# Optimization experiments

Measured on AMD Instinct MI355X. Metric: run time of the kernel, lower is better.

## Reference

```python
import jax, jax.numpy as jnp
import numpy as np

PAD = 0
NEG_INF = -1e30

B, P, Q, D = 32, 4096, 64, 128  # batch, passage len, question len, nhid


def setup_inputs() -> dict:
    key = jax.random.key(0)
    k1, k2, k3, k4, k5, k6 = jax.random.split(key, 6)
    return {
        "tensor_H": jax.random.normal(k1, (B, P, D), dtype=jnp.float32),
        "tensor_U": jax.random.normal(k2, (B, Q, D), dtype=jnp.float32),
        "M": jax.random.normal(k3, (B, P, D), dtype=jnp.float32),
        "sentence_word_rep": jax.random.randint(k4, (B, P), 0, 10000, dtype=jnp.int64),
        "W_attn": jax.random.normal(k5, (D, D), dtype=jnp.float32) / np.sqrt(D),
        "W_cls": jax.random.normal(k6, (5 * D, 2), dtype=jnp.float32) / np.sqrt(5 * D),
    }


def reference(tensor_H, tensor_U, M, sentence_word_rep, W_attn, W_cls):
    # Matrix attention (bilinear): S[b,p,q] = h_p^T W u_q  -> (B, P, Q)
    S = jnp.einsum("bpd,de,bqe->bpq", tensor_H, W_attn, tensor_U)
    # context-to-query: softmax over question axis, then bmm with U
    c2q = jnp.einsum("bpq,bqd->bpd", jax.nn.softmax(S, axis=2), tensor_U)
    # query-to-context: softmax over passage axis of row-max, weighted sum of H
    b_attn = jax.nn.softmax(jnp.max(S, axis=2), axis=-1)        # (B, P)
    q2c = jnp.einsum("bp,bpd->bd", b_attn, tensor_H)[:, None, :]  # (B, 1, D) broadcast over P
    # G = [H; c2q; H*c2q; H*q2c] -> (B, P, 4D); G_M = [G; M] -> (B, P, 5D)
    G_M = jnp.concatenate(
        [tensor_H, c2q, tensor_H * c2q, tensor_H * q2c, M], axis=2
    )
    # masked max-pool over passage positions (mask where token == PAD)
    pad_mask = (sentence_word_rep == PAD)[:, :, None]           # (B, P, 1)
    pooled = jnp.max(jnp.where(pad_mask, NEG_INF, G_M), axis=1)  # (B, 5D)
    # final linear classifier (no bias)
    return pooled @ W_cls                                        # (B, 2)
```

## Files before the change

### kernel.cpp

```cpp
#include <hip/hip_runtime.h>

#define B_ 32
#define P_ 4096
#define Q_ 64
#define D_ 128

#define PART_STRIDE 772
#define NCHUNK 32
#define CHUNK_ROWS 128
#define TWS_BYTES (96*16384)

typedef __attribute__((ext_vector_type(8))) short bf16x8;
typedef __attribute__((ext_vector_type(4))) float f32x4;

__device__ __forceinline__ unsigned int asu(float x) { return __float_as_uint(x); }
__device__ __forceinline__ float asf(unsigned int x) { return __uint_as_float(x); }

__global__ __launch_bounds__(256) void k_T(const float* __restrict__ U,
                                           const float* __restrict__ W,
                                           char* __restrict__ Tws) {
  __shared__ float Wl[128*132];
  __shared__ float Ul[8*128];
  const int b = blockIdx.x >> 3, qc = blockIdx.x & 7;
  const int t = threadIdx.x;
#pragma unroll
  for (int k = 0; k < 16; ++k) {
    int i = t*4 + k*1024;
    float4 wv = *(const float4*)(W + i);
    int d = i >> 7, e = i & 127;
    *(float4*)(&Wl[d*132 + e]) = wv;
  }
  {
    int i = t*4;
    int q = i >> 7, e = i & 127;
    *(float4*)(&Ul[q*128 + e]) =
        *(const float4*)(U + ((size_t)(b*Q_ + qc*8 + q))*D_ + e);
  }
  __syncthreads();
  const int d = t & 127, qhalf = t >> 7;
  char* Thi = Tws + b*16384;
  char* Tlo = Tws + 32*16384 + b*16384;
  char* Utl = Tws + 64*16384 + b*16384;
#pragma unroll
  for (int pass = 0; pass < 4; ++pass) {
    const int ql = pass*2 + qhalf;
    const int qg = qc*8 + ql;
    float acc = 0.f;
#pragma unroll
    for (int e = 0; e < 128; e += 4) {
      float4 wv = *(float4*)(&Wl[d*132 + e]);
      float4 uv = *(float4*)(&Ul[ql*128 + e]);
      acc += wv.x*uv.x + wv.y*uv.y + wv.z*uv.z + wv.w*uv.w;
    }
    unsigned int au = asu(acc);
    unsigned short hs = (unsigned short)(au >> 16);
    float lo = acc - asf(au & 0xFFFF0000u);
    unsigned short ls = (unsigned short)(asu(lo) >> 16);
    int ta = (qg*256 + 2*d) ^ ((qg & 7) << 4);
    *(unsigned short*)(Thi + ta) = hs;
    *(unsigned short*)(Tlo + ta) = ls;
    float uval = Ul[ql*128 + d];
    int ua = (d*128 + 2*qg) ^ ((d & 7) << 4);
    *(unsigned short*)(Utl + ua) = (unsigned short)(asu(uval) >> 16);
  }
}

__global__ __launch_bounds__(512, 8) void k_main(
    const float* __restrict__ H, const float* __restrict__ M,
    const int* __restrict__ tok, const char* __restrict__ Tws,
    float* __restrict__ part) {
  __shared__ __align__(16) char Pl[16384];
  __shared__ float mrow[128];
  __shared__ float rzrow[128];
  __shared__ float prow[128];
  __shared__ int   tkl[128];

  const int bid = blockIdx.x;
  const int b = bid >> 5, chunk = bid & 31;
  const int t = threadIdx.x, wv = t >> 6, l = t & 63;
  const int r15 = l & 15, g4 = l >> 4;
  const char* Thi = Tws + b*16384;
  const char* Tlo = Tws + 32*16384 + b*16384;
  const char* Utl = Tws + 64*16384 + b*16384;

  if (t < 128) tkl[t] = tok[b*P_ + chunk*CHUNK_ROWS + t];

  const int rowB = b*P_ + chunk*CHUNK_ROWS;

  {
    const int lrow0 = wv*16;
    f32x4 sacc[4];
#pragma unroll
    for (int qt = 0; qt < 4; ++qt) sacc[qt] = (f32x4){0.f, 0.f, 0.f, 0.f};
    const float* Arow = H + (size_t)(rowB + lrow0 + r15)*D_;
#pragma unroll
    for (int ks = 0; ks < 4; ++ks) {
      const float* ap = Arow + ks*32 + g4*8;
      float4 fa = *(const float4*)(ap);
      float4 fb = *(const float4*)(ap + 4);
      union { bf16x8 v; unsigned int u[4]; } Ah, Al;
      {
        unsigned int a0 = asu(fa.x), a1 = asu(fa.y), a2 = asu(fa.z), a3 = asu(fa.w);
        unsigned int c0 = asu(fb.x), c1 = asu(fb.y), c2 = asu(fb.z), c3 = asu(fb.w);
        Ah.u[0] = (a1 & 0xFFFF0000u) | (a0 >> 16);
        Ah.u[1] = (a3 & 0xFFFF0000u) | (a2 >> 16);
        Ah.u[2] = (c1 & 0xFFFF0000u) | (c0 >> 16);
        Ah.u[3] = (c3 & 0xFFFF0000u) | (c2 >> 16);
        float p0 = fa.x - asf(a0 & 0xFFFF0000u);
        float p1 = fa.y - asf(a1 & 0xFFFF0000u);
        float p2 = fa.z - asf(a2 & 0xFFFF0000u);
        float p3 = fa.w - asf(a3 & 0xFFFF0000u);
        float p4 = fb.x - asf(c0 & 0xFFFF0000u);
        float p5 = fb.y - asf(c1 & 0xFFFF0000u);
        float p6 = fb.z - asf(c2 & 0xFFFF0000u);
        float p7 = fb.w - asf(c3 & 0xFFFF0000u);
        Al.u[0] = (asu(p1) & 0xFFFF0000u) | (asu(p0) >> 16);
        Al.u[1] = (asu(p3) & 0xFFFF0000u) | (asu(p2) >> 16);
        Al.u[2] = (asu(p5) & 0xFFFF0000u) | (asu(p4) >> 16);
        Al.u[3] = (asu(p7) & 0xFFFF0000u) | (asu(p6) >> 16);
      }
#pragma unroll
      for (int qt = 0; qt < 4; ++qt) {
        int q = qt*16 + r15;
        int off = (q*256 + ks*64 + g4*16) ^ ((q & 7) << 4);
        bf16x8 bh = *(const bf16x8*)(Thi + off);
        bf16x8 bl = *(const bf16x8*)(Tlo + off);
        sacc[qt] = __builtin_amdgcn_mfma_f32_16x16x32_bf16(Al.v, bh, sacc[qt], 0, 0, 0);
        sacc[qt] = __builtin_amdgcn_mfma_f32_16x16x32_bf16(Ah.v, bl, sacc[qt], 0, 0, 0);
        sacc[qt] = __builtin_amdgcn_mfma_f32_16x16x32_bf16(Ah.v, bh, sacc[qt], 0, 0, 0);
      }
    }
    float m[4];
#pragma unroll
    for (int j = 0; j < 4; ++j)
      m[j] = fmaxf(fmaxf(sacc[0][j], sacc[1][j]), fmaxf(sacc[2][j], sacc[3][j]));
#pragma unroll
    for (int off = 1; off <= 8; off <<= 1)
#pragma unroll
      for (int j = 0; j < 4; ++j) m[j] = fmaxf(m[j], __shfl_xor(m[j], off));
    float Zp[4] = {0.f, 0.f, 0.f, 0.f};
#pragma unroll
    for (int qt = 0; qt < 4; ++qt)
#pragma unroll
      for (int j = 0; j < 4; ++j) {
        float e = __expf(sacc[qt][j] - m[j]);
        Zp[j] += e;
        int p = lrow0 + g4*4 + j, q = qt*16 + r15;
        int off = (p*128 + 2*q) ^ ((p & 7) << 4);
        *(unsigned short*)(Pl + off) = (unsigned short)(asu(e) >> 16);
      }
#pragma unroll
    for (int off = 1; off <= 8; off <<= 1)
#pragma unroll
      for (int j = 0; j < 4; ++j) Zp[j] += __shfl_xor(Zp[j], off);
    if (r15 == 0) {
#pragma unroll
      for (int j = 0; j < 4; ++j) {
        mrow[lrow0 + g4*4 + j]  = m[j];
        rzrow[lrow0 + g4*4 + j] = __builtin_amdgcn_rcpf(Zp[j]);
      }
    }
  }
  __syncthreads();

  float m0 = mrow[l], m1 = mrow[l + 64];
  float Lm = fmaxf(m0, m1);
#pragma unroll
  for (int off = 1; off <= 32; off <<= 1) Lm = fmaxf(Lm, __shfl_xor(Lm, off));
  float ssum = __expf(m0 - Lm) + __expf(m1 - Lm);
#pragma unroll
  for (int off = 1; off <= 32; off <<= 1) ssum += __shfl_xor(ssum, off);
  if (t < 128) prow[t] = __expf(mrow[t] - Lm);
  __syncthreads();

  const int dd = wv*16 + r15;
  bf16x8 bu0 = *(const bf16x8*)(Utl + ((dd*128 +  0 + g4*16) ^ ((dd & 7) << 4)));
  bf16x8 bu1 = *(const bf16x8*)(Utl + ((dd*128 + 64 + g4*16) ^ ((dd & 7) << 4)));

  float v = 0.f, xH = -3.0e38f, nH = 3.0e38f;
  float xC = -3.0e38f, xHC = -3.0e38f, xM = -3.0e38f;
#pragma unroll
  for (int rti = 0; rti < 8; ++rti) {
    const int rt = (rti + wv) & 7;
    f32x4 pv = (f32x4){0.f, 0.f, 0.f, 0.f};
    {
      int pr0 = rt*16 + r15;
      bf16x8 a0 = *(bf16x8*)(Pl + ((pr0*128 +  0 + g4*16) ^ ((r15 & 7) << 4)));
      bf16x8 a1 = *(bf16x8*)(Pl + ((pr0*128 + 64 + g4*16) ^ ((r15 & 7) << 4)));
      pv = __builtin_amdgcn_mfma_f32_16x16x32_bf16(a0, bu0, pv, 0, 0, 0);
      pv = __builtin_amdgcn_mfma_f32_16x16x32_bf16(a1, bu1, pv, 0, 0, 0);
    }
    const float* Hrow = H + (size_t)(rowB + rt*16 + g4*4)*D_ + dd;
    const float* Mrow = M + (size_t)(rowB + rt*16 + g4*4)*D_ + dd;
#pragma unroll
    for (int j = 0; j < 4; ++j) {
      const int row = rt*16 + g4*4 + j;
      const int tkv = tkl[row];
      const float bmax = tkv ? 0.f : -1.0e38f;
      const float bmin = tkv ? 0.f : 1.0e38f;
      float pr = prow[row];
      float h  = Hrow[(size_t)j*D_];
      float mv = Mrow[(size_t)j*D_];
      float c  = pv[j] * rzrow[row];
      v   += pr*h;
      xH   = fmaxf(xH,  h + bmax);
      nH   = fminf(nH,  h + bmin);
      xC   = fmaxf(xC,  c + bmax);
      xHC  = fmaxf(xHC, h*c + bmax);
      xM   = fmaxf(xM,  mv + bmax);
    }
  }
#pragma unroll
  for (int off = 16; off <= 32; off <<= 1) {
    v   += __shfl_xor(v, off);
    xH   = fmaxf(xH,  __shfl_xor(xH,  off));
    nH   = fminf(nH,  __shfl_xor(nH,  off));
    xC   = fmaxf(xC,  __shfl_xor(xC,  off));
    xHC  = fmaxf(xHC, __shfl_xor(xHC, off));
    xM   = fmaxf(xM,  __shfl_xor(xM,  off));
  }
  float* pp = part + (size_t)bid*PART_STRIDE;
  if (t == 0) { pp[0] = Lm; pp[1] = ssum; }
  if (g4 == 0) {
    pp[2 + dd]   = v;
    pp[130 + dd] = xH;
    pp[258 + dd] = nH;
    pp[386 + dd] = xC;
    pp[514 + dd] = xHC;
    pp[642 + dd] = xM;
  }
}

__global__ __launch_bounds__(128) void k_final(const float* __restrict__ part,
                                               const float* __restrict__ Wc,
                                               float* __restrict__ out) {
  __shared__ float pooled[640];
  __shared__ float r0s[2], r1s[2];
  const int b = blockIdx.x, t = threadIdx.x;
  const float* pb = part + (size_t)b*NCHUNK*PART_STRIDE;
  float L = -3.0e38f;
#pragma unroll
  for (int c = 0; c < NCHUNK; ++c) L = fmaxf(L, pb[c*PART_STRIDE]);
  float S = 0.f, V = 0.f;
  float mh = -3.0e38f, nh = 3.0e38f, mc = -3.0e38f, mhc = -3.0e38f, mm = -3.0e38f;
#pragma unroll
  for (int c = 0; c < NCHUNK; ++c) {
    const float* p = pb + c*PART_STRIDE;
    float e = __expf(p[0] - L);
    S += p[1]*e;
    V += p[2 + t]*e;
    mh  = fmaxf(mh,  p[130 + t]);
    nh  = fminf(nh,  p[258 + t]);
    mc  = fmaxf(mc,  p[386 + t]);
    mhc = fmaxf(mhc, p[514 + t]);
    mm  = fmaxf(mm,  p[642 + t]);
  }
  float q2c = V / S;
  pooled[t]       = mh;
  pooled[128 + t] = mc;
  pooled[256 + t] = mhc;
  pooled[384 + t] = (q2c >= 0.f) ? q2c*mh : q2c*nh;
  pooled[512 + t] = mm;
  __syncthreads();
  float a0 = 0.f, a1 = 0.f;
#pragma unroll
  for (int k = t; k < 640; k += 128) {
    float pv = pooled[k];
    a0 += pv*Wc[k*2 + 0];
    a1 += pv*Wc[k*2 + 1];
  }
#pragma unroll
  for (int off = 32; off; off >>= 1) {
    a0 += __shfl_xor(a0, off);
    a1 += __shfl_xor(a1, off);
  }
  if ((t & 63) == 0) { r0s[t >> 6] = a0; r1s[t >> 6] = a1; }
  __syncthreads();
  if (t == 0) {
    out[b*2 + 0] = r0s[0] + r0s[1];
    out[b*2 + 1] = r1s[0] + r1s[1];
  }
}

extern "C" void kernel_launch(void* const* d_in, const int* in_sizes, int n_in,
                              void* d_out, int out_size, void* d_ws, size_t ws_size,
                              hipStream_t stream) {
  const float* H   = (const float*)d_in[0];
  const float* U   = (const float*)d_in[1];
  const float* M   = (const float*)d_in[2];
  const int*   tok = (const int*)d_in[3];
  const float* Wa  = (const float*)d_in[4];
  const float* Wc  = (const float*)d_in[5];
  float* out = (float*)d_out;
  char* wsc = (char*)d_ws;
  char* Tws = wsc;
  float* part = (float*)(wsc + TWS_BYTES);

  hipLaunchKernelGGL(k_T,     dim3(256),        dim3(256), 0, stream, U, Wa, Tws);
  hipLaunchKernelGGL(k_main,  dim3(B_*NCHUNK),  dim3(512), 0, stream, H, M, tok, Tws, part);
  hipLaunchKernelGGL(k_final, dim3(B_),         dim3(128), 0, stream, part, Wc, out);
}
```

Baseline: 65.10 us.

## Halve chunk size to 64 rows, use 256-thread blocks with two d-columns per lane

Splits each batch's passage into 64 chunks of 64 rows, so twice as many blocks run with 256 threads each. In the second phase each lane now covers two output columns and reuses the same P fragments for two MFMAs. Per-row mask, probability and reciprocal values are precomputed into shared arrays and read as float4 vectors. The aim is better occupancy and more parallelism, at the cost of twice as many partial records for k_final to reduce.

```diff
diff --git a/kernel.cpp b/kernel.cpp
--- a/kernel.cpp
+++ b/kernel.cpp
@@ -6,8 +6,8 @@
 #define D_ 128
 
 #define PART_STRIDE 772
-#define NCHUNK 32
-#define CHUNK_ROWS 128
+#define NCHUNK 64
+#define CHUNK_ROWS 64
 #define TWS_BYTES (96*16384)
 
 typedef __attribute__((ext_vector_type(8))) short bf16x8;
@@ -65,55 +65,56 @@
   }
 }
 
-__global__ __launch_bounds__(512, 8) void k_main(
+__global__ __launch_bounds__(256, 8) void k_main(
     const float* __restrict__ H, const float* __restrict__ M,
     const int* __restrict__ tok, const char* __restrict__ Tws,
     float* __restrict__ part) {
-  __shared__ __align__(16) char Pl[16384];
-  __shared__ float mrow[128];
-  __shared__ float rzrow[128];
-  __shared__ float prow[128];
-  __shared__ int   tkl[128];
+  __shared__ __align__(16) char Pl[8192];
+  __shared__ __align__(16) float mrow[64];
+  __shared__ __align__(16) float rzrow[64];
+  __shared__ __align__(16) float prow[64];
+  __shared__ __align__(16) float bm[64];
+  __shared__ int tkl[64];
 
   const int bid = blockIdx.x;
-  const int b = bid >> 5, chunk = bid & 31;
+  const int b = bid >> 6, chunk = bid & 63;
   const int t = threadIdx.x, wv = t >> 6, l = t & 63;
   const int r15 = l & 15, g4 = l >> 4;
-  const char* Thi = Tws + b*16384;
-  const char* Tlo = Tws + 32*16384 + b*16384;
-  const char* Utl = Tws + 64*16384 + b*16384;
-
-  if (t < 128) tkl[t] = tok[b*P_ + chunk*CHUNK_ROWS + t];
+  const char* Thi_g = Tws + b*16384;
+  const char* Tlo_g = Tws + 32*16384 + b*16384;
+  const char* Utl   = Tws + 64*16384 + b*16384;
+
+  if (t < 64) tkl[t] = tok[b*P_ + chunk*CHUNK_ROWS + t];
 
   const int rowB = b*P_ + chunk*CHUNK_ROWS;
 
   {
     const int lrow0 = wv*16;
+    const float* Arow = H + (size_t)(rowB + lrow0 + r15)*D_;
     f32x4 sacc[4];
 #pragma unroll
     for (int qt = 0; qt < 4; ++qt) sacc[qt] = (f32x4){0.f, 0.f, 0.f, 0.f};
-    const float* Arow = H + (size_t)(rowB + lrow0 + r15)*D_;
 #pragma unroll
     for (int ks = 0; ks < 4; ++ks) {
       const float* ap = Arow + ks*32 + g4*8;
-      float4 fa = *(const float4*)(ap);
-      float4 fb = *(const float4*)(ap + 4);
+      f32x4 fa = *(const f32x4*)(ap);
+      f32x4 fb = *(const f32x4*)(ap + 4);
       union { bf16x8 v; unsigned int u[4]; } Ah, Al;
       {
-        unsigned int a0 = asu(fa.x), a1 = asu(fa.y), a2 = asu(fa.z), a3 = asu(fa.w);
-        unsigned int c0 = asu(fb.x), c1 = asu(fb.y), c2 = asu(fb.z), c3 = asu(fb.w);
+        unsigned int a0 = asu(fa[0]), a1 = asu(fa[1]), a2 = asu(fa[2]), a3 = asu(fa[3]);
+        unsigned int c0 = asu(fb[0]), c1 = asu(fb[1]), c2 = asu(fb[2]), c3 = asu(fb[3]);
         Ah.u[0] = (a1 & 0xFFFF0000u) | (a0 >> 16);
         Ah.u[1] = (a3 & 0xFFFF0000u) | (a2 >> 16);
         Ah.u[2] = (c1 & 0xFFFF0000u) | (c0 >> 16);
         Ah.u[3] = (c3 & 0xFFFF0000u) | (c2 >> 16);
-        float p0 = fa.x - asf(a0 & 0xFFFF0000u);
-        float p1 = fa.y - asf(a1 & 0xFFFF0000u);
-        float p2 = fa.z - asf(a2 & 0xFFFF0000u);
-        float p3 = fa.w - asf(a3 & 0xFFFF0000u);
-        float p4 = fb.x - asf(c0 & 0xFFFF0000u);
-        float p5 = fb.y - asf(c1 & 0xFFFF0000u);
-        float p6 = fb.z - asf(c2 & 0xFFFF0000u);
-        float p7 = fb.w - asf(c3 & 0xFFFF0000u);
+        float p0 = fa[0] - asf(a0 & 0xFFFF0000u);
+        float p1 = fa[1] - asf(a1 & 0xFFFF0000u);
+        float p2 = fa[2] - asf(a2 & 0xFFFF0000u);
+        float p3 = fa[3] - asf(a3 & 0xFFFF0000u);
+        float p4 = fb[0] - asf(c0 & 0xFFFF0000u);
+        float p5 = fb[1] - asf(c1 & 0xFFFF0000u);
+        float p6 = fb[2] - asf(c2 & 0xFFFF0000u);
+        float p7 = fb[3] - asf(c3 & 0xFFFF0000u);
         Al.u[0] = (asu(p1) & 0xFFFF0000u) | (asu(p0) >> 16);
         Al.u[1] = (asu(p3) & 0xFFFF0000u) | (asu(p2) >> 16);
         Al.u[2] = (asu(p5) & 0xFFFF0000u) | (asu(p4) >> 16);
@@ -123,8 +124,8 @@
       for (int qt = 0; qt < 4; ++qt) {
         int q = qt*16 + r15;
         int off = (q*256 + ks*64 + g4*16) ^ ((q & 7) << 4);
-        bf16x8 bh = *(const bf16x8*)(Thi + off);
-        bf16x8 bl = *(const bf16x8*)(Tlo + off);
+        bf16x8 bh = *(const bf16x8*)(Thi_g + off);
+        bf16x8 bl = *(const bf16x8*)(Tlo_g + off);
         sacc[qt] = __builtin_amdgcn_mfma_f32_16x16x32_bf16(Al.v, bh, sacc[qt], 0, 0, 0);
         sacc[qt] = __builtin_amdgcn_mfma_f32_16x16x32_bf16(Ah.v, bl, sacc[qt], 0, 0, 0);
         sacc[qt] = __builtin_amdgcn_mfma_f32_16x16x32_bf16(Ah.v, bh, sacc[qt], 0, 0, 0);
@@ -163,71 +164,86 @@
   }
   __syncthreads();
 
-  float m0 = mrow[l], m1 = mrow[l + 64];
-  float Lm = fmaxf(m0, m1);
+  float m0 = mrow[l];
+  float Lm = m0;
 #pragma unroll
   for (int off = 1; off <= 32; off <<= 1) Lm = fmaxf(Lm, __shfl_xor(Lm, off));
-  float ssum = __expf(m0 - Lm) + __expf(m1 - Lm);
+  float ssum = __expf(m0 - Lm);
 #pragma unroll
   for (int off = 1; off <= 32; off <<= 1) ssum += __shfl_xor(ssum, off);
-  if (t < 128) prow[t] = __expf(mrow[t] - Lm);
-  __syncthreads();
-
-  const int dd = wv*16 + r15;
-  bf16x8 bu0 = *(const bf16x8*)(Utl + ((dd*128 +  0 + g4*16) ^ ((dd & 7) << 4)));
-  bf16x8 bu1 = *(const bf16x8*)(Utl + ((dd*128 + 64 + g4*16) ^ ((dd & 7) << 4)));
-
-  float v = 0.f, xH = -3.0e38f, nH = 3.0e38f;
-  float xC = -3.0e38f, xHC = -3.0e38f, xM = -3.0e38f;
-#pragma unroll
-  for (int rti = 0; rti < 8; ++rti) {
-    const int rt = (rti + wv) & 7;
-    f32x4 pv = (f32x4){0.f, 0.f, 0.f, 0.f};
+  if (t < 64) {
+    prow[t] = __expf(mrow[t] - Lm);
+    bm[t]   = tkl[t] ? 0.f : -1.0e38f;
+  }
+  __syncthreads();
+
+  const int dd0 = wv*32 + r15;
+  const int dd1 = dd0 + 16;
+  bf16x8 bu00 = *(const bf16x8*)(Utl + ((dd0*128 +  0 + g4*16) ^ ((dd0 & 7) << 4)));
+  bf16x8 bu01 = *(const bf16x8*)(Utl + ((dd0*128 + 64 + g4*16) ^ ((dd0 & 7) << 4)));
+  bf16x8 bu10 = *(const bf16x8*)(Utl + ((dd1*128 +  0 + g4*16) ^ ((dd1 & 7) << 4)));
+  bf16x8 bu11 = *(const bf16x8*)(Utl + ((dd1*128 + 64 + g4*16) ^ ((dd1 & 7) << 4)));
+
+  float v0 = 0.f, v1 = 0.f;
+  float xH0 = -3.0e38f, xH1 = -3.0e38f, nH0 = 3.0e38f, nH1 = 3.0e38f;
+  float xC0 = -3.0e38f, xC1 = -3.0e38f, xHC0 = -3.0e38f, xHC1 = -3.0e38f;
+  float xM0 = -3.0e38f, xM1 = -3.0e38f;
+#pragma unroll
+  for (int rti = 0; rti < 4; ++rti) {
+    const int rt = (rti + wv) & 3;
+    f32x4 pv0 = (f32x4){0.f, 0.f, 0.f, 0.f};
+    f32x4 pv1 = (f32x4){0.f, 0.f, 0.f, 0.f};
     {
       int pr0 = rt*16 + r15;
       bf16x8 a0 = *(bf16x8*)(Pl + ((pr0*128 +  0 + g4*16) ^ ((r15 & 7) << 4)));
       bf16x8 a1 = *(bf16x8*)(Pl + ((pr0*128 + 64 + g4*16) ^ ((r15 & 7) << 4)));
-      pv = __builtin_amdgcn_mfma_f32_16x16x32_bf16(a0, bu0, pv, 0, 0, 0);
-      pv = __builtin_amdgcn_mfma_f32_16x16x32_bf16(a1, bu1, pv, 0, 0, 0);
-    }
-    const float* Hrow = H + (size_t)(rowB + rt*16 + g4*4)*D_ + dd;
-    const float* Mrow = M + (size_t)(rowB + rt*16 + g4*4)*D_ + dd;
+      pv0 = __builtin_amdgcn_mfma_f32_16x16x32_bf16(a0, bu00, pv0, 0, 0, 0);
+      pv0 = __builtin_amdgcn_mfma_f32_16x16x32_bf16(a1, bu01, pv0, 0, 0, 0);
+      pv1 = __builtin_amdgcn_mfma_f32_16x16x32_bf16(a0, bu10, pv1, 0, 0, 0);
+      pv1 = __builtin_amdgcn_mfma_f32_16x16x32_bf16(a1, bu11, pv1, 0, 0, 0);
+    }
+    const int rg = rt*16 + g4*4;
+    const float* Hrow = H + (size_t)(rowB + rg)*D_;
+    const float* Mrow = M + (size_t)(rowB + rg)*D_;
+    f32x4 prw = *(const f32x4*)&prow[rg];
+    f32x4 rzw = *(const f32x4*)&rzrow[rg];
+    f32x4 bmw = *(const f32x4*)&bm[rg];
 #pragma unroll
     for (int j = 0; j < 4; ++j) {
-      const int row = rt*16 + g4*4 + j;
-      const int tkv = tkl[row];
-      const float bmax = tkv ? 0.f : -1.0e38f;
-      const float bmin = tkv ? 0.f : 1.0e38f;
-      float pr = prow[row];
-      float h  = Hrow[(size_t)j*D_];
-      float mv = Mrow[(size_t)j*D_];
-      float c  = pv[j] * rzrow[row];
-      v   += pr*h;
-      xH   = fmaxf(xH,  h + bmax);
-      nH   = fminf(nH,  h + bmin);
-      xC   = fmaxf(xC,  c + bmax);
-      xHC  = fmaxf(xHC, h*c + bmax);
-      xM   = fmaxf(xM,  mv + bmax);
+      const float bmax = bmw[j];
+      const float bmin = -bmax;
+      float h0 = Hrow[(size_t)j*D_ + dd0];
+      float h1 = Hrow[(size_t)j*D_ + dd1];
+      float mv0 = Mrow[(size_t)j*D_ + dd0];
+      float mv1 = Mrow[(size_t)j*D_ + dd1];
+      float c0 = pv0[j] * rzw[j];
+      float c1 = pv1[j] * rzw[j];
+      v0   += prw[j]*h0;             v1   += prw[j]*h1;
+      xH0   = fmaxf(xH0,  h0 + bmax);  xH1   = fmaxf(xH1,  h1 + bmax);
+      nH0   = fminf(nH0,  h0 + bmin);  nH1   = fminf(nH1,  h1 + bmin);
+      xC0   = fmaxf(xC0,  c0 + bmax);  xC1   = fmaxf(xC1,  c1 + bmax);
+      xHC0  = fmaxf(xHC0, h0*c0 + bmax); xHC1 = fmaxf(xHC1, h1*c1 + bmax);
+      xM0   = fmaxf(xM0,  mv0 + bmax); xM1   = fmaxf(xM1,  mv1 + bmax);
     }
   }
 #pragma unroll
   for (int off = 16; off <= 32; off <<= 1) {
-    v   += __shfl_xor(v, off);
-    xH   = fmaxf(xH,  __shfl_xor(xH,  off));
-    nH   = fminf(nH,  __shfl_xor(nH,  off));
-    xC   = fmaxf(xC,  __shfl_xor(xC,  off));
-    xHC  = fmaxf(xHC, __shfl_xor(xHC, off));
-    xM   = fmaxf(xM,  __shfl_xor(xM,  off));
+    v0   += __shfl_xor(v0, off);            v1   += __shfl_xor(v1, off);
+    xH0   = fmaxf(xH0,  __shfl_xor(xH0,  off)); xH1 = fmaxf(xH1, __shfl_xor(xH1, off));
+    nH0   = fminf(nH0,  __shfl_xor(nH0,  off)); nH1 = fminf(nH1, __shfl_xor(nH1, off));
+    xC0   = fmaxf(xC0,  __shfl_xor(xC0,  off)); xC1 = fmaxf(xC1, __shfl_xor(xC1, off));
+    xHC0  = fmaxf(xHC0, __shfl_xor(xHC0, off)); xHC1 = fmaxf(xHC1, __shfl_xor(xHC1, off));
+    xM0   = fmaxf(xM0,  __shfl_xor(xM0,  off)); xM1 = fmaxf(xM1, __shfl_xor(xM1, off));
   }
   float* pp = part + (size_t)bid*PART_STRIDE;
   if (t == 0) { pp[0] = Lm; pp[1] = ssum; }
   if (g4 == 0) {
-    pp[2 + dd]   = v;
-    pp[130 + dd] = xH;
-    pp[258 + dd] = nH;
-    pp[386 + dd] = xC;
-    pp[514 + dd] = xHC;
-    pp[642 + dd] = xM;
+    pp[2 + dd0]   = v0;    pp[2 + dd1]   = v1;
+    pp[130 + dd0] = xH0;   pp[130 + dd1] = xH1;
+    pp[258 + dd0] = nH0;   pp[258 + dd1] = nH1;
+    pp[386 + dd0] = xC0;   pp[386 + dd1] = xC1;
+    pp[514 + dd0] = xHC0;  pp[514 + dd1] = xHC1;
+    pp[642 + dd0] = xM0;   pp[642 + dd1] = xM1;
   }
 }
 
@@ -297,6 +313,6 @@
   float* part = (float*)(wsc + TWS_BYTES);
 
   hipLaunchKernelGGL(k_T,     dim3(256),        dim3(256), 0, stream, U, Wa, Tws);
-  hipLaunchKernelGGL(k_main,  dim3(B_*NCHUNK),  dim3(512), 0, stream, H, M, tok, Tws, part);
+  hipLaunchKernelGGL(k_main,  dim3(B_*NCHUNK),  dim3(256), 0, stream, H, M, tok, Tws, part);
   hipLaunchKernelGGL(k_final, dim3(B_),         dim3(128), 0, stream, part, Wc, out);
 }
```

Result: slower. 120.0 us (+84.4%).
